# Performance work log

Measured on AMD Instinct MI355X. Metric: run time of the kernel, lower is better.

Reference implementation:

```python
import jax, jax.numpy as jnp
import numpy as np

H = 512          # hidden_dim
T = 20           # output_seq_len
EPS = 1e-5


def _ln(x, g, b):
    m = jnp.mean(x, axis=-1, keepdims=True)
    v = jnp.mean((x - m) ** 2, axis=-1, keepdims=True)
    return (x - m) * jax.lax.rsqrt(v + EPS) * g + b


def setup_inputs() -> dict:
    key = jax.random.key(0)
    ks = jax.random.split(key, 20)
    N, LD, PD = 65536, 128, 32
    s = 0.02
    return {
        "z_q": jax.random.normal(ks[0], (N, LD), jnp.float32),
        "f_prior": jax.random.normal(ks[1], (N, PD), jnp.float32),
        # init_mlp: Linear(160 -> 1024) -> LN -> GELU -> Linear(1024 -> 512) -> Tanh
        "W1": jax.random.normal(ks[2], (LD + PD, 2 * H), jnp.float32) * s,
        "b1": jnp.zeros((2 * H,), jnp.float32),
        "g1": jnp.ones((2 * H,), jnp.float32),
        "be1": jnp.zeros((2 * H,), jnp.float32),
        "W2": jax.random.normal(ks[3], (2 * H, H), jnp.float32) * s,
        "b2": jnp.zeros((H,), jnp.float32),
        # start token (output_dim = 1)
        "start_token": jax.random.normal(ks[4], (1,), jnp.float32) * 0.1,
        # GRU, input_size=1, hidden_size=H, gates stacked [r, z, n] (torch layout)
        "W_ih": jax.random.normal(ks[5], (3 * H, 1), jnp.float32) * s,
        "W_hh": jax.random.normal(ks[6], (3 * H, H), jnp.float32) * s,
        "b_ih": jnp.zeros((3 * H,), jnp.float32),
        "b_hh": jnp.zeros((3 * H,), jnp.float32),
        # output_mlp: Linear(H -> H//2) -> LN -> GELU -> Linear(H//2 -> 1)
        "Wo1": jax.random.normal(ks[7], (H, H // 2), jnp.float32) * s,
        "bo1": jnp.zeros((H // 2,), jnp.float32),
        "go": jnp.ones((H // 2,), jnp.float32),
        "beo": jnp.zeros((H // 2,), jnp.float32),
        "Wo2": jax.random.normal(ks[8], (H // 2, 1), jnp.float32) * s,
        "bo2": jnp.zeros((1,), jnp.float32),
    }


def reference(z_q, f_prior, W1, b1, g1, be1, W2, b2, start_token,
              W_ih, W_hh, b_ih, b_hh, Wo1, bo1, go, beo, Wo2, bo2):
    N = z_q.shape[0]
    # init_mlp -> h_0 (dropout is identity at eval)
    combined = jnp.concatenate([z_q, f_prior], axis=1)          # (N, LD+PD)
    h = jnp.tanh(jax.nn.gelu(_ln(combined @ W1 + b1, g1, be1), approximate=False) @ W2 + b2)  # (N, H)

    x0 = jnp.broadcast_to(start_token[None, :], (N, 1))          # (N, 1)

    def step(carry, _):
        h, x = carry
        gi = x @ W_ih.T + b_ih                                   # (N, 3H)
        gh = h @ W_hh.T + b_hh                                   # (N, 3H)
        r = jax.nn.sigmoid(gi[:, :H] + gh[:, :H])
        z = jax.nn.sigmoid(gi[:, H:2 * H] + gh[:, H:2 * H])
        n = jnp.tanh(gi[:, 2 * H:] + r * gh[:, 2 * H:])
        h_new = (1.0 - z) * n + z * h
        y = jax.nn.gelu(_ln(h_new @ Wo1 + bo1, go, beo), approximate=False) @ Wo2 + bo2  # (N, 1)
        return (h_new, y), y

    _, ys = jax.lax.scan(step, (h, x0), None, length=T)          # (T, N, 1)
    preds = jnp.transpose(ys[..., 0], (1, 0))                    # (N, T), output_dim==1 squeeze
    return preds
```

## Files before the change

kernel.cpp:

```cpp
#include <hip/hip_runtime.h>
#include <math.h>


typedef _Float16 f16;
typedef _Float16 f16x4 __attribute__((ext_vector_type(4)));
typedef _Float16 f16x8 __attribute__((ext_vector_type(8)));
typedef float f32x4 __attribute__((ext_vector_type(4)));

#define TSTEPS 20

__device__ __forceinline__ float sigm(float v) { return 1.0f / (1.0f + __expf(-v)); }
__device__ __forceinline__ float tanh_s(float v) {
  float e = __expf(-2.0f * fabsf(v));
  float r = (1.0f - e) / (1.0f + e);
  return copysignf(r, v);
}
__device__ __forceinline__ float gelu_e(float v) {
  return 0.5f * v * (1.0f + erff(v * 0.70710678118654752f));
}
__device__ __forceinline__ void st4(float* d, float4 v) {
  d[0] = v.x; d[1] = v.y; d[2] = v.z; d[3] = v.w;
}

__device__ __forceinline__ int fa(int m, int k) {
  return (((k >> 5) * 4 + (m >> 4)) << 10) + (((m & 15) + ((k >> 3) & 3) * 16) << 4) + ((k & 7) * 2);
}

__global__ void cvt_weights(const float* __restrict__ W1, const float* __restrict__ W2,
                            const float* __restrict__ Whh, const float* __restrict__ Wo1,
                            const float* __restrict__ bih, const float* __restrict__ bhh,
                            f16* __restrict__ w1t, f16* __restrict__ w2t,
                            f16* __restrict__ whh, f16* __restrict__ wo1t,
                            float* __restrict__ bcr, float* __restrict__ bcz) {
  int i = blockIdx.x * 256 + threadIdx.x;
  if (i < 163840) { int n = i / 160; int k = i - n * 160; w1t[i] = (f16)W1[k * 1024 + n]; return; }
  i -= 163840;
  if (i < 524288) { int n = i >> 10; int k = i & 1023; w2t[i] = (f16)W2[k * 512 + n]; return; }
  i -= 524288;
  if (i < 786432) { whh[i] = (f16)Whh[i]; return; }
  i -= 786432;
  if (i < 131072) { int o = i >> 9; int k = i & 511; wo1t[i] = (f16)Wo1[k * 256 + o]; return; }
  i -= 131072;
  if (i < 512) { bcr[i] = bih[i] + bhh[i]; return; }
  i -= 512;
  if (i < 512) { bcz[i] = bih[512 + i] + bhh[512 + i]; return; }
}

__global__ __launch_bounds__(512, 2)
void gru_main(
    const float* __restrict__ zq, const float* __restrict__ fpr,
    const float* __restrict__ b1, const float* __restrict__ g1, const float* __restrict__ be1,
    const float* __restrict__ b2, const float* __restrict__ stok,
    const float* __restrict__ Wih, const float* __restrict__ bih, const float* __restrict__ bhh,
    const float* __restrict__ bo1, const float* __restrict__ go, const float* __restrict__ beo,
    const float* __restrict__ Wo2, const float* __restrict__ bo2,
    const f16* __restrict__ w1t, const f16* __restrict__ w2t,
    const f16* __restrict__ whh, const f16* __restrict__ wo1t,
    const float* __restrict__ bcr, const float* __restrict__ bcz,
    float* __restrict__ out) {
  __shared__ __align__(16) unsigned char sm[131072];
  __shared__ float sm_s[256], sm_ss[256], sm_yp[256];
  __shared__ float sm_x[64];

  const int tid = threadIdx.x;
  const int w = tid >> 6;
  const int lane = tid & 63;
  const int l16 = lane & 15;
  const int l4 = lane >> 4;
  const int R0 = blockIdx.x * 64;

  const float bo2v = bo2[0];
  if (tid < 64) sm_x[tid] = stok[0];

  #pragma unroll 1
  for (int p = 0; p < 4; ++p) {
    #pragma unroll 1
    for (int jh = 0; jh < 2; ++jh) {
      const int jq0 = w * 128 + p * 32 + jh * 16;
      f32x4 acc[4];
      #pragma unroll
      for (int mt = 0; mt < 4; ++mt) acc[mt] = (f32x4){0.f, 0.f, 0.f, 0.f};
      #pragma unroll
      for (int kf = 0; kf < 5; ++kf) {
        const int k0 = kf * 32 + l4 * 8;
        f16x8 B[4];
        #pragma unroll
        for (int mt = 0; mt < 4; ++mt) {
          const int gm = R0 + mt * 16 + l16;
          const float* src = (kf < 4) ? (zq + gm * 128 + k0) : (fpr + gm * 32 + (k0 - 128));
          float4 v0 = *(const float4*)src;
          float4 v1 = *(const float4*)(src + 4);
          f16x8 b;
          b[0] = (f16)v0.x; b[1] = (f16)v0.y; b[2] = (f16)v0.z; b[3] = (f16)v0.w;
          b[4] = (f16)v1.x; b[5] = (f16)v1.y; b[6] = (f16)v1.z; b[7] = (f16)v1.w;
          B[mt] = b;
        }
        const f16x8 A = *(const f16x8*)(w1t + (jq0 + l16) * 160 + k0);
        #pragma unroll
        for (int mt = 0; mt < 4; ++mt)
          acc[mt] = __builtin_amdgcn_mfma_f32_16x16x32_f16(A, B[mt], acc[mt], 0, 0, 0);
      }
      const int jq = jq0 + l4 * 4;
      float bb[4]; st4(bb, *(const float4*)(b1 + jq));
      #pragma unroll
      for (int mt = 0; mt < 4; ++mt) {
        f16x4 v;
        #pragma unroll
        for (int r = 0; r < 4; ++r) v[r] = (f16)(acc[mt][r] + bb[r]);
        *(f16x4*)(sm + fa(mt * 16 + l16, jq)) = v;
      }
    }
  }
  __syncthreads();
  {
    const int mt = w & 3, half = w >> 2;
    const int row = mt * 16 + l16;
    float s = 0.f, ss = 0.f;
    #pragma unroll 4
    for (int it = 0; it < 16; ++it) {
      const int kb = half * 16 + it;
      f16x8 v = *(const f16x8*)(sm + (kb * 4 + mt) * 1024 + lane * 16);
      #pragma unroll
      for (int i = 0; i < 8; ++i) { float f = (float)v[i]; s += f; ss += f * f; }
    }
    s += __shfl_xor(s, 16); ss += __shfl_xor(ss, 16);
    s += __shfl_xor(s, 32); ss += __shfl_xor(ss, 32);
    if (l4 == 0) { sm_s[row * 2 + half] = s; sm_ss[row * 2 + half] = ss; }
    __syncthreads();
    const float mean = (sm_s[row * 2] + sm_s[row * 2 + 1]) * (1.f / 1024.f);
    const float q2 = (sm_ss[row * 2] + sm_ss[row * 2 + 1]) * (1.f / 1024.f);
    const float rstd = rsqrtf(q2 - mean * mean + 1e-5f);
    #pragma unroll 2
    for (int it = 0; it < 16; ++it) {
      const int kb = half * 16 + it;
      const int off = (kb * 4 + mt) * 1024 + lane * 16;
      const int c = kb * 32 + l4 * 8;
      f16x8 v = *(const f16x8*)(sm + off);
      float4 ga = *(const float4*)(g1 + c);
      float4 gb = *(const float4*)(g1 + c + 4);
      float4 ba = *(const float4*)(be1 + c);
      float4 bb = *(const float4*)(be1 + c + 4);
      float gs[8] = {ga.x, ga.y, ga.z, ga.w, gb.x, gb.y, gb.z, gb.w};
      float bs[8] = {ba.x, ba.y, ba.z, ba.w, bb.x, bb.y, bb.z, bb.w};
      f16x8 o;
      #pragma unroll
      for (int i = 0; i < 8; ++i)
        o[i] = (f16)gelu_e(((float)v[i] - mean) * rstd * gs[i] + bs[i]);
      *(f16x8*)(sm + off) = o;
    }
  }
  __syncthreads();
  f16x4 hold[4][4];
  #pragma unroll 1
  for (int pp = 0; pp < 4; ++pp) {
    const int jq0 = w * 64 + pp * 16;
    f32x4 acc[4];
    #pragma unroll
    for (int mt = 0; mt < 4; ++mt) acc[mt] = (f32x4){0.f, 0.f, 0.f, 0.f};
    #pragma unroll 2
    for (int kf = 0; kf < 32; ++kf) {
      f16x8 B[4];
      #pragma unroll
      for (int mt = 0; mt < 4; ++mt)
        B[mt] = *(const f16x8*)(sm + (kf * 4 + mt) * 1024 + lane * 16);
      const f16x8 A = *(const f16x8*)(w2t + (jq0 + l16) * 1024 + kf * 32 + l4 * 8);
      #pragma unroll
      for (int mt = 0; mt < 4; ++mt)
        acc[mt] = __builtin_amdgcn_mfma_f32_16x16x32_f16(A, B[mt], acc[mt], 0, 0, 0);
    }
    const int jq = jq0 + l4 * 4;
    float bb[4]; st4(bb, *(const float4*)(b2 + jq));
    #pragma unroll
    for (int mt = 0; mt < 4; ++mt) {
      f16x4 v;
      #pragma unroll
      for (int r = 0; r < 4; ++r) v[r] = (f16)tanh_s(acc[mt][r] + bb[r]);
      hold[pp][mt] = v;
    }
  }
  __syncthreads();
  #pragma unroll
  for (int pp = 0; pp < 4; ++pp) {
    const int jq = w * 64 + pp * 16 + l4 * 4;
    #pragma unroll
    for (int mt = 0; mt < 4; ++mt)
      *(f16x4*)(sm + fa(mt * 16 + l16, jq)) = hold[pp][mt];
  }
  __syncthreads();

  #pragma unroll 1
  for (int t = 0; t < TSTEPS; ++t) {
    const int cur = (t & 1) << 16;
    const int nxt = cur ^ 65536;
    #pragma unroll 1
    for (int p = 0; p < 2; ++p) {
      f32x4 acc[4][3][2];
      #pragma unroll
      for (int mt = 0; mt < 4; ++mt)
        #pragma unroll
        for (int g = 0; g < 3; ++g)
          #pragma unroll
          for (int jh = 0; jh < 2; ++jh) acc[mt][g][jh] = (f32x4){0.f, 0.f, 0.f, 0.f};
      #pragma unroll 2
      for (int kf = 0; kf < 16; ++kf) {
        f16x8 B[4];
        #pragma unroll
        for (int mt = 0; mt < 4; ++mt)
          B[mt] = *(const f16x8*)(sm + cur + (kf * 4 + mt) * 1024 + lane * 16);
        #pragma unroll
        for (int g = 0; g < 3; ++g)
          #pragma unroll
          for (int jh = 0; jh < 2; ++jh) {
            const f16x8 A = *(const f16x8*)(whh + (g * 512 + w * 64 + p * 32 + jh * 16 + l16) * 512 + kf * 32 + l4 * 8);
            #pragma unroll
            for (int mt = 0; mt < 4; ++mt)
              acc[mt][g][jh] = __builtin_amdgcn_mfma_f32_16x16x32_f16(A, B[mt], acc[mt][g][jh], 0, 0, 0);
          }
      }
      if (p == 0) __syncthreads();
      #pragma unroll
      for (int jh = 0; jh < 2; ++jh) {
        const int jq = w * 64 + p * 32 + jh * 16 + l4 * 4;
        float wr[4], wz[4], wn[4], cr[4], cz[4], bn[4], cn[4];
        st4(wr, *(const float4*)(Wih + jq));
        st4(wz, *(const float4*)(Wih + 512 + jq));
        st4(wn, *(const float4*)(Wih + 1024 + jq));
        st4(cr, *(const float4*)(bcr + jq));
        st4(cz, *(const float4*)(bcz + jq));
        st4(bn, *(const float4*)(bih + 1024 + jq));
        st4(cn, *(const float4*)(bhh + 1024 + jq));
        #pragma unroll
        for (int mt = 0; mt < 4; ++mt) {
          const int m = mt * 16 + l16;
          const float x = sm_x[m];
          const int hoff = fa(m, jq);
          const f16x4 ho = *(const f16x4*)(sm + cur + hoff);
          f16x4 hn;
          #pragma unroll
          for (int r = 0; r < 4; ++r) {
            const float gr = sigm(x * wr[r] + cr[r] + acc[mt][0][jh][r]);
            const float gz = sigm(x * wz[r] + cz[r] + acc[mt][1][jh][r]);
            const float gn = tanh_s(x * wn[r] + bn[r] + gr * (acc[mt][2][jh][r] + cn[r]));
            hn[r] = (f16)((1.f - gz) * gn + gz * (float)ho[r]);
          }
          *(f16x4*)(sm + nxt + hoff) = hn;
        }
      }
    }
    __syncthreads();
    {
      const int mg = w >> 2, jg = w & 3;
      f32x4 a2[2][4];
      #pragma unroll
      for (int mi = 0; mi < 2; ++mi)
        #pragma unroll
        for (int jt2 = 0; jt2 < 4; ++jt2) a2[mi][jt2] = (f32x4){0.f, 0.f, 0.f, 0.f};
      #pragma unroll 2
      for (int kf = 0; kf < 16; ++kf) {
        f16x8 B[2];
        #pragma unroll
        for (int mi = 0; mi < 2; ++mi)
          B[mi] = *(const f16x8*)(sm + nxt + (kf * 4 + mg * 2 + mi) * 1024 + lane * 16);
        #pragma unroll
        for (int jt2 = 0; jt2 < 4; ++jt2) {
          const f16x8 A = *(const f16x8*)(wo1t + (jg * 64 + jt2 * 16 + l16) * 512 + kf * 32 + l4 * 8);
          #pragma unroll
          for (int mi = 0; mi < 2; ++mi)
            a2[mi][jt2] = __builtin_amdgcn_mfma_f32_16x16x32_f16(A, B[mi], a2[mi][jt2], 0, 0, 0);
        }
      }
      float vv[2][4][4];
      float bo1v[4][4];
      #pragma unroll
      for (int jt2 = 0; jt2 < 4; ++jt2)
        st4(bo1v[jt2], *(const float4*)(bo1 + jg * 64 + jt2 * 16 + l4 * 4));
      #pragma unroll
      for (int mi = 0; mi < 2; ++mi) {
        float s = 0.f, ss = 0.f;
        #pragma unroll
        for (int jt2 = 0; jt2 < 4; ++jt2)
          #pragma unroll
          for (int r = 0; r < 4; ++r) {
            const float v = a2[mi][jt2][r] + bo1v[jt2][r];
            vv[mi][jt2][r] = v; s += v; ss += v * v;
          }
        s += __shfl_xor(s, 16); ss += __shfl_xor(ss, 16);
        s += __shfl_xor(s, 32); ss += __shfl_xor(ss, 32);
        if (l4 == 0) {
          const int m = (mg * 2 + mi) * 16 + l16;
          sm_s[m * 4 + jg] = s;
          sm_ss[m * 4 + jg] = ss;
        }
      }
      __syncthreads();
      float gov[4][4], bev[4][4], wv[4][4];
      #pragma unroll
      for (int jt2 = 0; jt2 < 4; ++jt2) {
        const int jb = jg * 64 + jt2 * 16 + l4 * 4;
        st4(gov[jt2], *(const float4*)(go + jb));
        st4(bev[jt2], *(const float4*)(beo + jb));
        st4(wv[jt2], *(const float4*)(Wo2 + jb));
      }
      #pragma unroll
      for (int mi = 0; mi < 2; ++mi) {
        const int m = (mg * 2 + mi) * 16 + l16;
        float4 ps = *(const float4*)(sm_s + m * 4);
        float4 pq = *(const float4*)(sm_ss + m * 4);
        const float mean = (ps.x + ps.y + ps.z + ps.w) * (1.f / 256.f);
        const float q2 = (pq.x + pq.y + pq.z + pq.w) * (1.f / 256.f);
        const float rstd = rsqrtf(q2 - mean * mean + 1e-5f);
        float y = 0.f;
        #pragma unroll
        for (int jt2 = 0; jt2 < 4; ++jt2)
          #pragma unroll
          for (int r = 0; r < 4; ++r)
            y += gelu_e((vv[mi][jt2][r] - mean) * rstd * gov[jt2][r] + bev[jt2][r]) * wv[jt2][r];
        y += __shfl_xor(y, 16);
        y += __shfl_xor(y, 32);
        if (l4 == 0) sm_yp[m * 4 + jg] = y;
      }
      __syncthreads();
      if (tid < 64) {
        float4 ps = *(const float4*)(sm_yp + tid * 4);
        const float y = bo2v + ps.x + ps.y + ps.z + ps.w;
        sm_x[tid] = y;
        out[(R0 + tid) * 20 + t] = y;
      }
    }
  }
}

extern "C" void kernel_launch(void* const* d_in, const int* in_sizes, int n_in,
                              void* d_out, int out_size, void* d_ws, size_t ws_size,
                              hipStream_t stream) {
  const float* zq   = (const float*)d_in[0];
  const float* fpr  = (const float*)d_in[1];
  const float* W1   = (const float*)d_in[2];
  const float* b1   = (const float*)d_in[3];
  const float* g1   = (const float*)d_in[4];
  const float* be1  = (const float*)d_in[5];
  const float* W2   = (const float*)d_in[6];
  const float* b2   = (const float*)d_in[7];
  const float* stok = (const float*)d_in[8];
  const float* Wih  = (const float*)d_in[9];
  const float* Whh  = (const float*)d_in[10];
  const float* bih  = (const float*)d_in[11];
  const float* bhh  = (const float*)d_in[12];
  const float* Wo1  = (const float*)d_in[13];
  const float* bo1  = (const float*)d_in[14];
  const float* go   = (const float*)d_in[15];
  const float* beo  = (const float*)d_in[16];
  const float* Wo2  = (const float*)d_in[17];
  const float* bo2  = (const float*)d_in[18];

  char* ws = (char*)d_ws;
  f16* w1t   = (f16*)(ws + 0);
  f16* w2t   = (f16*)(ws + 327680);
  f16* whh   = (f16*)(ws + 1376256);
  f16* wo1t  = (f16*)(ws + 2949120);
  float* bcr = (float*)(ws + 3211264);
  float* bcz = (float*)(ws + 3213312);

  cvt_weights<<<6276, 256, 0, stream>>>(W1, W2, Whh, Wo1, bih, bhh,
                                        w1t, w2t, whh, wo1t, bcr, bcz);

  const int N = in_sizes[0] / 128;
  gru_main<<<N / 64, 512, 0, stream>>>(zq, fpr, b1, g1, be1, b2, stok, Wih, bih, bhh,
                                       bo1, go, beo, Wo2, bo2, w1t, w2t, whh, wo1t,
                                       bcr, bcz, (float*)d_out);
}
```

Measured before the change: 5.997 ms.

## Halve shared memory by splitting init MLP into row halves and single-buffering h

After: 7.707 ms. 1.29x slower.

```diff
diff --git a/kernel.cpp b/kernel.cpp
--- a/kernel.cpp
+++ b/kernel.cpp
@@ -25,13 +25,17 @@
 __device__ __forceinline__ int fa(int m, int k) {
   return (((k >> 5) * 4 + (m >> 4)) << 10) + (((m & 15) + ((k >> 3) & 3) * 16) << 4) + ((k & 7) * 2);
 }
+__device__ __forceinline__ int fa32(int m, int k) {
+  return (((k >> 5) * 2 + ((m >> 4) & 1)) << 10) + (((m & 15) + ((k >> 3) & 3) * 16) << 4) + ((k & 7) * 2);
+}
 
 __global__ void cvt_weights(const float* __restrict__ W1, const float* __restrict__ W2,
                             const float* __restrict__ Whh, const float* __restrict__ Wo1,
-                            const float* __restrict__ bih, const float* __restrict__ bhh,
+                            const float* __restrict__ Wih, const float* __restrict__ bih,
+                            const float* __restrict__ bhh,
                             f16* __restrict__ w1t, f16* __restrict__ w2t,
                             f16* __restrict__ whh, f16* __restrict__ wo1t,
-                            float* __restrict__ bcr, float* __restrict__ bcz) {
+                            f16* __restrict__ c7) {
   int i = blockIdx.x * 256 + threadIdx.x;
   if (i < 163840) { int n = i / 160; int k = i - n * 160; w1t[i] = (f16)W1[k * 1024 + n]; return; }
   i -= 163840;
@@ -41,9 +45,18 @@
   i -= 786432;
   if (i < 131072) { int o = i >> 9; int k = i & 511; wo1t[i] = (f16)Wo1[k * 256 + o]; return; }
   i -= 131072;
-  if (i < 512) { bcr[i] = bih[i] + bhh[i]; return; }
-  i -= 512;
-  if (i < 512) { bcz[i] = bih[512 + i] + bhh[512 + i]; return; }
+  if (i < 3584) {
+    const int which = i >> 9, j = i & 511;
+    float v;
+    if (which == 0) v = Wih[j];
+    else if (which == 1) v = Wih[512 + j];
+    else if (which == 2) v = Wih[1024 + j];
+    else if (which == 3) v = bih[j] + bhh[j];
+    else if (which == 4) v = bih[512 + j] + bhh[512 + j];
+    else if (which == 5) v = bih[1024 + j];
+    else v = bhh[1024 + j];
+    c7[i] = (f16)v;
+  }
 }
 
 __global__ __launch_bounds__(512, 2)
@@ -51,14 +64,13 @@
     const float* __restrict__ zq, const float* __restrict__ fpr,
     const float* __restrict__ b1, const float* __restrict__ g1, const float* __restrict__ be1,
     const float* __restrict__ b2, const float* __restrict__ stok,
-    const float* __restrict__ Wih, const float* __restrict__ bih, const float* __restrict__ bhh,
     const float* __restrict__ bo1, const float* __restrict__ go, const float* __restrict__ beo,
     const float* __restrict__ Wo2, const float* __restrict__ bo2,
     const f16* __restrict__ w1t, const f16* __restrict__ w2t,
     const f16* __restrict__ whh, const f16* __restrict__ wo1t,
-    const float* __restrict__ bcr, const float* __restrict__ bcz,
+    const f16* __restrict__ c7,
     float* __restrict__ out) {
-  __shared__ __align__(16) unsigned char sm[131072];
+  __shared__ __align__(16) unsigned char sm[65536];
   __shared__ float sm_s[256], sm_ss[256], sm_yp[256];
   __shared__ float sm_x[64];
 
@@ -72,180 +84,199 @@
   const float bo2v = bo2[0];
   if (tid < 64) sm_x[tid] = stok[0];
 
-  #pragma unroll 1
-  for (int p = 0; p < 4; ++p) {
+  f16x4 h0h[2][4][2];
+
+  #pragma unroll
+  for (int hh = 0; hh < 2; ++hh) {
+    const int RH = R0 + hh * 32;
     #pragma unroll 1
-    for (int jh = 0; jh < 2; ++jh) {
-      const int jq0 = w * 128 + p * 32 + jh * 16;
-      f32x4 acc[4];
-      #pragma unroll
-      for (int mt = 0; mt < 4; ++mt) acc[mt] = (f32x4){0.f, 0.f, 0.f, 0.f};
-      #pragma unroll
-      for (int kf = 0; kf < 5; ++kf) {
-        const int k0 = kf * 32 + l4 * 8;
-        f16x8 B[4];
-        #pragma unroll
-        for (int mt = 0; mt < 4; ++mt) {
-          const int gm = R0 + mt * 16 + l16;
-          const float* src = (kf < 4) ? (zq + gm * 128 + k0) : (fpr + gm * 32 + (k0 - 128));
-          float4 v0 = *(const float4*)src;
-          float4 v1 = *(const float4*)(src + 4);
-          f16x8 b;
-          b[0] = (f16)v0.x; b[1] = (f16)v0.y; b[2] = (f16)v0.z; b[3] = (f16)v0.w;
-          b[4] = (f16)v1.x; b[5] = (f16)v1.y; b[6] = (f16)v1.z; b[7] = (f16)v1.w;
-          B[mt] = b;
-        }
-        const f16x8 A = *(const f16x8*)(w1t + (jq0 + l16) * 160 + k0);
-        #pragma unroll
-        for (int mt = 0; mt < 4; ++mt)
+    for (int p = 0; p < 4; ++p) {
+      #pragma unroll 1
+      for (int jh = 0; jh < 2; ++jh) {
+        const int jq0 = w * 128 + p * 32 + jh * 16;
+        f32x4 acc[2];
+        #pragma unroll
+        for (int mt = 0; mt < 2; ++mt) acc[mt] = (f32x4){0.f, 0.f, 0.f, 0.f};
+        #pragma unroll
+        for (int kf = 0; kf < 5; ++kf) {
+          const int k0 = kf * 32 + l4 * 8;
+          f16x8 B[2];
+          #pragma unroll
+          for (int mt = 0; mt < 2; ++mt) {
+            const int gm = RH + mt * 16 + l16;
+            const float* src = (kf < 4) ? (zq + gm * 128 + k0) : (fpr + gm * 32 + (k0 - 128));
+            float4 v0 = *(const float4*)src;
+            float4 v1 = *(const float4*)(src + 4);
+            f16x8 b;
+            b[0] = (f16)v0.x; b[1] = (f16)v0.y; b[2] = (f16)v0.z; b[3] = (f16)v0.w;
+            b[4] = (f16)v1.x; b[5] = (f16)v1.y; b[6] = (f16)v1.z; b[7] = (f16)v1.w;
+            B[mt] = b;
+          }
+          const f16x8 A = *(const f16x8*)(w1t + (jq0 + l16) * 160 + k0);
+          #pragma unroll
+          for (int mt = 0; mt < 2; ++mt)
+            acc[mt] = __builtin_amdgcn_mfma_f32_16x16x32_f16(A, B[mt], acc[mt], 0, 0, 0);
+        }
+        const int jq = jq0 + l4 * 4;
+        float bb[4]; st4(bb, *(const float4*)(b1 + jq));
+        #pragma unroll
+        for (int mt = 0; mt < 2; ++mt) {
+          f16x4 v;
+          #pragma unroll
+          for (int r = 0; r < 4; ++r) v[r] = (f16)(acc[mt][r] + bb[r]);
+          *(f16x4*)(sm + fa32(mt * 16 + l16, jq)) = v;
+        }
+      }
+    }
+    __syncthreads();
+    {
+      float s0 = 0.f, q0 = 0.f, s1 = 0.f, q1 = 0.f;
+      #pragma unroll
+      for (int i = 0; i < 8; ++i) {
+        f16x8 v = *(const f16x8*)(sm + (w * 8 + i) * 1024 + lane * 16);
+        float ls = 0.f, lq = 0.f;
+        #pragma unroll
+        for (int j = 0; j < 8; ++j) { float f = (float)v[j]; ls += f; lq += f * f; }
+        if (i & 1) { s1 += ls; q1 += lq; } else { s0 += ls; q0 += lq; }
+      }
+      s0 += __shfl_xor(s0, 16); q0 += __shfl_xor(q0, 16);
+      s0 += __shfl_xor(s0, 32); q0 += __shfl_xor(q0, 32);
+      s1 += __shfl_xor(s1, 16); q1 += __shfl_xor(q1, 16);
+      s1 += __shfl_xor(s1, 32); q1 += __shfl_xor(q1, 32);
+      if (l4 == 0) {
+        sm_s[l16 * 8 + w] = s0;        sm_ss[l16 * 8 + w] = q0;
+        sm_s[(16 + l16) * 8 + w] = s1; sm_ss[(16 + l16) * 8 + w] = q1;
+      }
+      __syncthreads();
+      float mean[2], rstd[2];
+      #pragma unroll
+      for (int mt = 0; mt < 2; ++mt) {
+        const int row = mt * 16 + l16;
+        float s = 0.f, q = 0.f;
+        #pragma unroll
+        for (int i = 0; i < 8; ++i) { s += sm_s[row * 8 + i]; q += sm_ss[row * 8 + i]; }
+        mean[mt] = s * (1.f / 1024.f);
+        rstd[mt] = rsqrtf(q * (1.f / 1024.f) - mean[mt] * mean[mt] + 1e-5f);
+      }
+      #pragma unroll 2
+      for (int i = 0; i < 8; ++i) {
+        const int chunk = w * 8 + i;
+        const int off = chunk * 1024 + lane * 16;
+        const int c = (chunk >> 1) * 32 + l4 * 8;
+        const int mt = i & 1;
+        f16x8 v = *(const f16x8*)(sm + off);
+        float4 ga = *(const float4*)(g1 + c);
+        float4 gb = *(const float4*)(g1 + c + 4);
+        float4 ba = *(const float4*)(be1 + c);
+        float4 bb = *(const float4*)(be1 + c + 4);
+        float gs[8] = {ga.x, ga.y, ga.z, ga.w, gb.x, gb.y, gb.z, gb.w};
+        float bs[8] = {ba.x, ba.y, ba.z, ba.w, bb.x, bb.y, bb.z, bb.w};
+        f16x8 o;
+        #pragma unroll
+        for (int j = 0; j < 8; ++j)
+          o[j] = (f16)gelu_e(((float)v[j] - mean[mt]) * rstd[mt] * gs[j] + bs[j]);
+        *(f16x8*)(sm + off) = o;
+      }
+    }
+    __syncthreads();
+    #pragma unroll
+    for (int pp = 0; pp < 4; ++pp) {
+      const int jq0 = w * 64 + pp * 16;
+      f32x4 acc[2];
+      #pragma unroll
+      for (int mt = 0; mt < 2; ++mt) acc[mt] = (f32x4){0.f, 0.f, 0.f, 0.f};
+      #pragma unroll 2
+      for (int kf = 0; kf < 32; ++kf) {
+        f16x8 B[2];
+        #pragma unroll
+        for (int mt = 0; mt < 2; ++mt)
+          B[mt] = *(const f16x8*)(sm + (kf * 2 + mt) * 1024 + lane * 16);
+        const f16x8 A = *(const f16x8*)(w2t + (jq0 + l16) * 1024 + kf * 32 + l4 * 8);
+        #pragma unroll
+        for (int mt = 0; mt < 2; ++mt)
           acc[mt] = __builtin_amdgcn_mfma_f32_16x16x32_f16(A, B[mt], acc[mt], 0, 0, 0);
       }
       const int jq = jq0 + l4 * 4;
-      float bb[4]; st4(bb, *(const float4*)(b1 + jq));
-      #pragma unroll
-      for (int mt = 0; mt < 4; ++mt) {
+      float bb[4]; st4(bb, *(const float4*)(b2 + jq));
+      #pragma unroll
+      for (int mt = 0; mt < 2; ++mt) {
         f16x4 v;
         #pragma unroll
-        for (int r = 0; r < 4; ++r) v[r] = (f16)(acc[mt][r] + bb[r]);
-        *(f16x4*)(sm + fa(mt * 16 + l16, jq)) = v;
-      }
-    }
+        for (int r = 0; r < 4; ++r) v[r] = (f16)tanh_s(acc[mt][r] + bb[r]);
+        h0h[hh][pp][mt] = v;
+      }
+    }
+    __syncthreads();
   }
-  __syncthreads();
-  {
-    const int mt = w & 3, half = w >> 2;
-    const int row = mt * 16 + l16;
-    float s = 0.f, ss = 0.f;
-    #pragma unroll 4
-    for (int it = 0; it < 16; ++it) {
-      const int kb = half * 16 + it;
-      f16x8 v = *(const f16x8*)(sm + (kb * 4 + mt) * 1024 + lane * 16);
-      #pragma unroll
-      for (int i = 0; i < 8; ++i) { float f = (float)v[i]; s += f; ss += f * f; }
-    }
-    s += __shfl_xor(s, 16); ss += __shfl_xor(ss, 16);
-    s += __shfl_xor(s, 32); ss += __shfl_xor(ss, 32);
-    if (l4 == 0) { sm_s[row * 2 + half] = s; sm_ss[row * 2 + half] = ss; }
-    __syncthreads();
-    const float mean = (sm_s[row * 2] + sm_s[row * 2 + 1]) * (1.f / 1024.f);
-    const float q2 = (sm_ss[row * 2] + sm_ss[row * 2 + 1]) * (1.f / 1024.f);
-    const float rstd = rsqrtf(q2 - mean * mean + 1e-5f);
-    #pragma unroll 2
-    for (int it = 0; it < 16; ++it) {
-      const int kb = half * 16 + it;
-      const int off = (kb * 4 + mt) * 1024 + lane * 16;
-      const int c = kb * 32 + l4 * 8;
-      f16x8 v = *(const f16x8*)(sm + off);
-      float4 ga = *(const float4*)(g1 + c);
-      float4 gb = *(const float4*)(g1 + c + 4);
-      float4 ba = *(const float4*)(be1 + c);
-      float4 bb = *(const float4*)(be1 + c + 4);
-      float gs[8] = {ga.x, ga.y, ga.z, ga.w, gb.x, gb.y, gb.z, gb.w};
-      float bs[8] = {ba.x, ba.y, ba.z, ba.w, bb.x, bb.y, bb.z, bb.w};
-      f16x8 o;
-      #pragma unroll
-      for (int i = 0; i < 8; ++i)
-        o[i] = (f16)gelu_e(((float)v[i] - mean) * rstd * gs[i] + bs[i]);
-      *(f16x8*)(sm + off) = o;
-    }
-  }
-  __syncthreads();
-  f16x4 hold[4][4];
-  #pragma unroll 1
-  for (int pp = 0; pp < 4; ++pp) {
-    const int jq0 = w * 64 + pp * 16;
-    f32x4 acc[4];
+  #pragma unroll
+  for (int hh = 0; hh < 2; ++hh)
     #pragma unroll
-    for (int mt = 0; mt < 4; ++mt) acc[mt] = (f32x4){0.f, 0.f, 0.f, 0.f};
-    #pragma unroll 2
-    for (int kf = 0; kf < 32; ++kf) {
-      f16x8 B[4];
-      #pragma unroll
-      for (int mt = 0; mt < 4; ++mt)
-        B[mt] = *(const f16x8*)(sm + (kf * 4 + mt) * 1024 + lane * 16);
-      const f16x8 A = *(const f16x8*)(w2t + (jq0 + l16) * 1024 + kf * 32 + l4 * 8);
-      #pragma unroll
-      for (int mt = 0; mt < 4; ++mt)
-        acc[mt] = __builtin_amdgcn_mfma_f32_16x16x32_f16(A, B[mt], acc[mt], 0, 0, 0);
-    }
-    const int jq = jq0 + l4 * 4;
-    float bb[4]; st4(bb, *(const float4*)(b2 + jq));
-    #pragma unroll
-    for (int mt = 0; mt < 4; ++mt) {
-      f16x4 v;
-      #pragma unroll
-      for (int r = 0; r < 4; ++r) v[r] = (f16)tanh_s(acc[mt][r] + bb[r]);
-      hold[pp][mt] = v;
-    }
-  }
-  __syncthreads();
-  #pragma unroll
-  for (int pp = 0; pp < 4; ++pp) {
-    const int jq = w * 64 + pp * 16 + l4 * 4;
-    #pragma unroll
-    for (int mt = 0; mt < 4; ++mt)
-      *(f16x4*)(sm + fa(mt * 16 + l16, jq)) = hold[pp][mt];
-  }
+    for (int pp = 0; pp < 4; ++pp) {
+      const int jq = w * 64 + pp * 16 + l4 * 4;
+      #pragma unroll
+      for (int mt = 0; mt < 2; ++mt)
+        *(f16x4*)(sm + fa(hh * 32 + mt * 16 + l16, jq)) = h0h[hh][pp][mt];
+    }
   __syncthreads();
 
   #pragma unroll 1
   for (int t = 0; t < TSTEPS; ++t) {
-    const int cur = (t & 1) << 16;
-    const int nxt = cur ^ 65536;
-    #pragma unroll 1
-    for (int p = 0; p < 2; ++p) {
-      f32x4 acc[4][3][2];
+    f16x4 hnh[4][4];
+    #pragma unroll
+    for (int q = 0; q < 4; ++q) {
+      const int jt = w * 64 + q * 16;
+      f32x4 acc[4][3];
       #pragma unroll
       for (int mt = 0; mt < 4; ++mt)
         #pragma unroll
-        for (int g = 0; g < 3; ++g)
-          #pragma unroll
-          for (int jh = 0; jh < 2; ++jh) acc[mt][g][jh] = (f32x4){0.f, 0.f, 0.f, 0.f};
+        for (int g = 0; g < 3; ++g) acc[mt][g] = (f32x4){0.f, 0.f, 0.f, 0.f};
       #pragma unroll 2
       for (int kf = 0; kf < 16; ++kf) {
         f16x8 B[4];
         #pragma unroll
         for (int mt = 0; mt < 4; ++mt)
-          B[mt] = *(const f16x8*)(sm + cur + (kf * 4 + mt) * 1024 + lane * 16);
-        #pragma unroll
-        for (int g = 0; g < 3; ++g)
-          #pragma unroll
-          for (int jh = 0; jh < 2; ++jh) {
-            const f16x8 A = *(const f16x8*)(whh + (g * 512 + w * 64 + p * 32 + jh * 16 + l16) * 512 + kf * 32 + l4 * 8);
-            #pragma unroll
-            for (int mt = 0; mt < 4; ++mt)
-              acc[mt][g][jh] = __builtin_amdgcn_mfma_f32_16x16x32_f16(A, B[mt], acc[mt][g][jh], 0, 0, 0);
-          }
-      }
-      if (p == 0) __syncthreads();
-      #pragma unroll
-      for (int jh = 0; jh < 2; ++jh) {
-        const int jq = w * 64 + p * 32 + jh * 16 + l4 * 4;
-        float wr[4], wz[4], wn[4], cr[4], cz[4], bn[4], cn[4];
-        st4(wr, *(const float4*)(Wih + jq));
-        st4(wz, *(const float4*)(Wih + 512 + jq));
-        st4(wn, *(const float4*)(Wih + 1024 + jq));
-        st4(cr, *(const float4*)(bcr + jq));
-        st4(cz, *(const float4*)(bcz + jq));
-        st4(bn, *(const float4*)(bih + 1024 + jq));
-        st4(cn, *(const float4*)(bhh + 1024 + jq));
-        #pragma unroll
-        for (int mt = 0; mt < 4; ++mt) {
-          const int m = mt * 16 + l16;
-          const float x = sm_x[m];
-          const int hoff = fa(m, jq);
-          const f16x4 ho = *(const f16x4*)(sm + cur + hoff);
-          f16x4 hn;
-          #pragma unroll
-          for (int r = 0; r < 4; ++r) {
-            const float gr = sigm(x * wr[r] + cr[r] + acc[mt][0][jh][r]);
-            const float gz = sigm(x * wz[r] + cz[r] + acc[mt][1][jh][r]);
-            const float gn = tanh_s(x * wn[r] + bn[r] + gr * (acc[mt][2][jh][r] + cn[r]));
-            hn[r] = (f16)((1.f - gz) * gn + gz * (float)ho[r]);
-          }
-          *(f16x4*)(sm + nxt + hoff) = hn;
-        }
-      }
+          B[mt] = *(const f16x8*)(sm + (kf * 4 + mt) * 1024 + lane * 16);
+        #pragma unroll
+        for (int g = 0; g < 3; ++g) {
+          const f16x8 A = *(const f16x8*)(whh + (g * 512 + jt + l16) * 512 + kf * 32 + l4 * 8);
+          #pragma unroll
+          for (int mt = 0; mt < 4; ++mt)
+            acc[mt][g] = __builtin_amdgcn_mfma_f32_16x16x32_f16(A, B[mt], acc[mt][g], 0, 0, 0);
+        }
+      }
+      if (q == 0) __syncthreads();
+      const int jq = jt + l4 * 4;
+      const f16x4 wrh = *(const f16x4*)(c7 + jq);
+      const f16x4 wzh = *(const f16x4*)(c7 + 512 + jq);
+      const f16x4 wnh = *(const f16x4*)(c7 + 1024 + jq);
+      const f16x4 crh = *(const f16x4*)(c7 + 1536 + jq);
+      const f16x4 czh = *(const f16x4*)(c7 + 2048 + jq);
+      const f16x4 bnh = *(const f16x4*)(c7 + 2560 + jq);
+      const f16x4 cnh = *(const f16x4*)(c7 + 3072 + jq);
+      #pragma unroll
+      for (int mt = 0; mt < 4; ++mt) {
+        const int m = mt * 16 + l16;
+        const float x = sm_x[m];
+        const int hoff = fa(m, jq);
+        const f16x4 ho = *(const f16x4*)(sm + hoff);
+        f16x4 hn;
+        #pragma unroll
+        for (int r = 0; r < 4; ++r) {
+          const float gr = sigm(x * (float)wrh[r] + (float)crh[r] + acc[mt][0][r]);
+          const float gz = sigm(x * (float)wzh[r] + (float)czh[r] + acc[mt][1][r]);
+          const float gn = tanh_s(x * (float)wnh[r] + (float)bnh[r] + gr * (acc[mt][2][r] + (float)cnh[r]));
+          hn[r] = (f16)((1.f - gz) * gn + gz * (float)ho[r]);
+        }
+        hnh[q][mt] = hn;
+      }
+    }
+    __syncthreads();
+    #pragma unroll
+    for (int q = 0; q < 4; ++q) {
+      const int jq = w * 64 + q * 16 + l4 * 4;
+      #pragma unroll
+      for (int mt = 0; mt < 4; ++mt)
+        *(f16x4*)(sm + fa(mt * 16 + l16, jq)) = hnh[q][mt];
     }
     __syncthreads();
     {
@@ -260,7 +291,7 @@
         f16x8 B[2];
         #pragma unroll
         for (int mi = 0; mi < 2; ++mi)
-          B[mi] = *(const f16x8*)(sm + nxt + (kf * 4 + mg * 2 + mi) * 1024 + lane * 16);
+          B[mi] = *(const f16x8*)(sm + (kf * 4 + mg * 2 + mi) * 1024 + lane * 16);
         #pragma unroll
         for (int jt2 = 0; jt2 < 4; ++jt2) {
           const f16x8 A = *(const f16x8*)(wo1t + (jg * 64 + jt2 * 16 + l16) * 512 + kf * 32 + l4 * 8);
@@ -354,18 +385,17 @@
   const float* bo2  = (const float*)d_in[18];
 
   char* ws = (char*)d_ws;
-  f16* w1t   = (f16*)(ws + 0);
-  f16* w2t   = (f16*)(ws + 327680);
-  f16* whh   = (f16*)(ws + 1376256);
-  f16* wo1t  = (f16*)(ws + 2949120);
-  float* bcr = (float*)(ws + 3211264);
-  float* bcz = (float*)(ws + 3213312);
-
-  cvt_weights<<<6276, 256, 0, stream>>>(W1, W2, Whh, Wo1, bih, bhh,
-                                        w1t, w2t, whh, wo1t, bcr, bcz);
+  f16* w1t  = (f16*)(ws + 0);
+  f16* w2t  = (f16*)(ws + 327680);
+  f16* whh  = (f16*)(ws + 1376256);
+  f16* wo1t = (f16*)(ws + 2949120);
+  f16* c7   = (f16*)(ws + 3211264);
+
+  cvt_weights<<<6287, 256, 0, stream>>>(W1, W2, Whh, Wo1, Wih, bih, bhh,
+                                        w1t, w2t, whh, wo1t, c7);
 
   const int N = in_sizes[0] / 128;
-  gru_main<<<N / 64, 512, 0, stream>>>(zq, fpr, b1, g1, be1, b2, stok, Wih, bih, bhh,
-                                       bo1, go, beo, Wo2, bo2, w1t, w2t, whh, wo1t,
-                                       bcr, bcz, (float*)d_out);
-}
+  gru_main<<<N / 64, 512, 0, stream>>>(zq, fpr, b1, g1, be1, b2, stok,
+                                       bo1, go, beo, Wo2, bo2,
+                                       w1t, w2t, whh, wo1t, c7, (float*)d_out);
+}
```

## Prefetch MFMA weight fragments one k-step ahead and stage GRU constants in LDS

Applied to the files above, without the earlier changes.

Measured after the change: 5.262 ms. 1.14x faster.

```diff
diff --git a/kernel.cpp b/kernel.cpp
--- a/kernel.cpp
+++ b/kernel.cpp
@@ -28,10 +28,11 @@
 
 __global__ void cvt_weights(const float* __restrict__ W1, const float* __restrict__ W2,
                             const float* __restrict__ Whh, const float* __restrict__ Wo1,
-                            const float* __restrict__ bih, const float* __restrict__ bhh,
+                            const float* __restrict__ Wih, const float* __restrict__ bih,
+                            const float* __restrict__ bhh,
                             f16* __restrict__ w1t, f16* __restrict__ w2t,
                             f16* __restrict__ whh, f16* __restrict__ wo1t,
-                            float* __restrict__ bcr, float* __restrict__ bcz) {
+                            f16* __restrict__ c7) {
   int i = blockIdx.x * 256 + threadIdx.x;
   if (i < 163840) { int n = i / 160; int k = i - n * 160; w1t[i] = (f16)W1[k * 1024 + n]; return; }
   i -= 163840;
@@ -41,9 +42,18 @@
   i -= 786432;
   if (i < 131072) { int o = i >> 9; int k = i & 511; wo1t[i] = (f16)Wo1[k * 256 + o]; return; }
   i -= 131072;
-  if (i < 512) { bcr[i] = bih[i] + bhh[i]; return; }
-  i -= 512;
-  if (i < 512) { bcz[i] = bih[512 + i] + bhh[512 + i]; return; }
+  if (i < 3584) {
+    const int which = i >> 9, j = i & 511;
+    float v;
+    if (which == 0) v = Wih[j];
+    else if (which == 1) v = Wih[512 + j];
+    else if (which == 2) v = Wih[1024 + j];
+    else if (which == 3) v = bih[j] + bhh[j];
+    else if (which == 4) v = bih[512 + j] + bhh[512 + j];
+    else if (which == 5) v = bih[1024 + j];
+    else v = bhh[1024 + j];
+    c7[i] = (f16)v;
+  }
 }
 
 __global__ __launch_bounds__(512, 2)
@@ -51,16 +61,17 @@
     const float* __restrict__ zq, const float* __restrict__ fpr,
     const float* __restrict__ b1, const float* __restrict__ g1, const float* __restrict__ be1,
     const float* __restrict__ b2, const float* __restrict__ stok,
-    const float* __restrict__ Wih, const float* __restrict__ bih, const float* __restrict__ bhh,
     const float* __restrict__ bo1, const float* __restrict__ go, const float* __restrict__ beo,
     const float* __restrict__ Wo2, const float* __restrict__ bo2,
     const f16* __restrict__ w1t, const f16* __restrict__ w2t,
     const f16* __restrict__ whh, const f16* __restrict__ wo1t,
-    const float* __restrict__ bcr, const float* __restrict__ bcz,
+    const f16* __restrict__ c7,
     float* __restrict__ out) {
   __shared__ __align__(16) unsigned char sm[131072];
   __shared__ float sm_s[256], sm_ss[256], sm_yp[256];
   __shared__ float sm_x[64];
+  __shared__ __align__(8) f16 sm_c7[3584];
+  __shared__ __align__(16) float sm_aux[1024];
 
   const int tid = threadIdx.x;
   const int w = tid >> 6;
@@ -71,6 +82,10 @@
 
   const float bo2v = bo2[0];
   if (tid < 64) sm_x[tid] = stok[0];
+  for (int i = tid; i < 1792; i += 512)
+    ((unsigned*)sm_c7)[i] = ((const unsigned*)c7)[i];
+  for (int i = tid; i < 1024; i += 512)
+    sm_aux[i] = (i < 256) ? bo1[i] : (i < 512) ? go[i - 256] : (i < 768) ? beo[i - 512] : Wo2[i - 768];
 
   #pragma unroll 1
   for (int p = 0; p < 4; ++p) {
@@ -144,31 +159,45 @@
       float bs[8] = {ba.x, ba.y, ba.z, ba.w, bb.x, bb.y, bb.z, bb.w};
       f16x8 o;
       #pragma unroll
-      for (int i = 0; i < 8; ++i)
-        o[i] = (f16)gelu_e(((float)v[i] - mean) * rstd * gs[i] + bs[i]);
+      for (int j = 0; j < 8; ++j)
+        o[j] = (f16)gelu_e(((float)v[j] - mean) * rstd * gs[j] + bs[j]);
       *(f16x8*)(sm + off) = o;
     }
   }
   __syncthreads();
   f16x4 hold[4][4];
-  #pragma unroll 1
+  #pragma unroll
   for (int pp = 0; pp < 4; ++pp) {
-    const int jq0 = w * 64 + pp * 16;
+    const f16* Ab = w2t + (w * 64 + pp * 16 + l16) * 1024 + l4 * 8;
     f32x4 acc[4];
     #pragma unroll
     for (int mt = 0; mt < 4; ++mt) acc[mt] = (f32x4){0.f, 0.f, 0.f, 0.f};
-    #pragma unroll 2
-    for (int kf = 0; kf < 32; ++kf) {
-      f16x8 B[4];
-      #pragma unroll
-      for (int mt = 0; mt < 4; ++mt)
-        B[mt] = *(const f16x8*)(sm + (kf * 4 + mt) * 1024 + lane * 16);
-      const f16x8 A = *(const f16x8*)(w2t + (jq0 + l16) * 1024 + kf * 32 + l4 * 8);
-      #pragma unroll
-      for (int mt = 0; mt < 4; ++mt)
-        acc[mt] = __builtin_amdgcn_mfma_f32_16x16x32_f16(A, B[mt], acc[mt], 0, 0, 0);
-    }
-    const int jq = jq0 + l4 * 4;
+    f16x8 A0 = *(const f16x8*)(Ab);
+    f16x8 A1 = *(const f16x8*)(Ab + 32);
+    #pragma unroll 1
+    for (int kp = 0; kp < 16; ++kp) {
+      {
+        f16x8 B[4];
+        #pragma unroll
+        for (int mt = 0; mt < 4; ++mt)
+          B[mt] = *(const f16x8*)(sm + ((kp * 8 + mt) << 10) + lane * 16);
+        #pragma unroll
+        for (int mt = 0; mt < 4; ++mt)
+          acc[mt] = __builtin_amdgcn_mfma_f32_16x16x32_f16(A0, B[mt], acc[mt], 0, 0, 0);
+        if (kp < 15) A0 = *(const f16x8*)(Ab + (kp * 2 + 2) * 32);
+      }
+      {
+        f16x8 B[4];
+        #pragma unroll
+        for (int mt = 0; mt < 4; ++mt)
+          B[mt] = *(const f16x8*)(sm + ((kp * 8 + 4 + mt) << 10) + lane * 16);
+        #pragma unroll
+        for (int mt = 0; mt < 4; ++mt)
+          acc[mt] = __builtin_amdgcn_mfma_f32_16x16x32_f16(A1, B[mt], acc[mt], 0, 0, 0);
+        if (kp < 15) A1 = *(const f16x8*)(Ab + (kp * 2 + 3) * 32);
+      }
+    }
+    const int jq = w * 64 + pp * 16 + l4 * 4;
     float bb[4]; st4(bb, *(const float4*)(b2 + jq));
     #pragma unroll
     for (int mt = 0; mt < 4; ++mt) {
@@ -193,87 +222,134 @@
     const int cur = (t & 1) << 16;
     const int nxt = cur ^ 65536;
     #pragma unroll 1
-    for (int p = 0; p < 2; ++p) {
-      f32x4 acc[4][3][2];
+    for (int q = 0; q < 4; ++q) {
+      const int jt = w * 64 + q * 16;
+      const f16* Ab = whh + (jt + l16) * 512 + l4 * 8;
+      f32x4 acc[4][3];
       #pragma unroll
       for (int mt = 0; mt < 4; ++mt)
         #pragma unroll
-        for (int g = 0; g < 3; ++g)
-          #pragma unroll
-          for (int jh = 0; jh < 2; ++jh) acc[mt][g][jh] = (f32x4){0.f, 0.f, 0.f, 0.f};
-      #pragma unroll 2
-      for (int kf = 0; kf < 16; ++kf) {
-        f16x8 B[4];
-        #pragma unroll
-        for (int mt = 0; mt < 4; ++mt)
-          B[mt] = *(const f16x8*)(sm + cur + (kf * 4 + mt) * 1024 + lane * 16);
-        #pragma unroll
-        for (int g = 0; g < 3; ++g)
-          #pragma unroll
-          for (int jh = 0; jh < 2; ++jh) {
-            const f16x8 A = *(const f16x8*)(whh + (g * 512 + w * 64 + p * 32 + jh * 16 + l16) * 512 + kf * 32 + l4 * 8);
+        for (int g = 0; g < 3; ++g) acc[mt][g] = (f32x4){0.f, 0.f, 0.f, 0.f};
+      f16x8 A0[3], A1[3];
+      #pragma unroll
+      for (int g = 0; g < 3; ++g) A0[g] = *(const f16x8*)(Ab + g * 262144);
+      #pragma unroll
+      for (int g = 0; g < 3; ++g) A1[g] = *(const f16x8*)(Ab + g * 262144 + 32);
+      #pragma unroll 1
+      for (int kp = 0; kp < 8; ++kp) {
+        {
+          f16x8 B[4];
+          #pragma unroll
+          for (int mt = 0; mt < 4; ++mt)
+            B[mt] = *(const f16x8*)(sm + cur + ((kp * 8 + mt) << 10) + lane * 16);
+          #pragma unroll
+          for (int g = 0; g < 3; ++g)
             #pragma unroll
             for (int mt = 0; mt < 4; ++mt)
-              acc[mt][g][jh] = __builtin_amdgcn_mfma_f32_16x16x32_f16(A, B[mt], acc[mt][g][jh], 0, 0, 0);
+              acc[mt][g] = __builtin_amdgcn_mfma_f32_16x16x32_f16(A0[g], B[mt], acc[mt][g], 0, 0, 0);
+          if (kp < 7) {
+            #pragma unroll
+            for (int g = 0; g < 3; ++g)
+              A0[g] = *(const f16x8*)(Ab + g * 262144 + (kp * 2 + 2) * 32);
           }
-      }
-      if (p == 0) __syncthreads();
-      #pragma unroll
-      for (int jh = 0; jh < 2; ++jh) {
-        const int jq = w * 64 + p * 32 + jh * 16 + l4 * 4;
-        float wr[4], wz[4], wn[4], cr[4], cz[4], bn[4], cn[4];
-        st4(wr, *(const float4*)(Wih + jq));
-        st4(wz, *(const float4*)(Wih + 512 + jq));
-        st4(wn, *(const float4*)(Wih + 1024 + jq));
-        st4(cr, *(const float4*)(bcr + jq));
-        st4(cz, *(const float4*)(bcz + jq));
-        st4(bn, *(const float4*)(bih + 1024 + jq));
-        st4(cn, *(const float4*)(bhh + 1024 + jq));
-        #pragma unroll
-        for (int mt = 0; mt < 4; ++mt) {
-          const int m = mt * 16 + l16;
-          const float x = sm_x[m];
-          const int hoff = fa(m, jq);
-          const f16x4 ho = *(const f16x4*)(sm + cur + hoff);
-          f16x4 hn;
-          #pragma unroll
-          for (int r = 0; r < 4; ++r) {
-            const float gr = sigm(x * wr[r] + cr[r] + acc[mt][0][jh][r]);
-            const float gz = sigm(x * wz[r] + cz[r] + acc[mt][1][jh][r]);
-            const float gn = tanh_s(x * wn[r] + bn[r] + gr * (acc[mt][2][jh][r] + cn[r]));
-            hn[r] = (f16)((1.f - gz) * gn + gz * (float)ho[r]);
+        }
+        {
+          f16x8 B[4];
+          #pragma unroll
+          for (int mt = 0; mt < 4; ++mt)
+            B[mt] = *(const f16x8*)(sm + cur + ((kp * 8 + 4 + mt) << 10) + lane * 16);
+          #pragma unroll
+          for (int g = 0; g < 3; ++g)
+            #pragma unroll
+            for (int mt = 0; mt < 4; ++mt)
+              acc[mt][g] = __builtin_amdgcn_mfma_f32_16x16x32_f16(A1[g], B[mt], acc[mt][g], 0, 0, 0);
+          if (kp < 7) {
+            #pragma unroll
+            for (int g = 0; g < 3; ++g)
+              A1[g] = *(const f16x8*)(Ab + g * 262144 + (kp * 2 + 3) * 32);
           }
-          *(f16x4*)(sm + nxt + hoff) = hn;
-        }
+        }
+      }
+      if (q == 0) __syncthreads();
+      const int jq = jt + l4 * 4;
+      const f16x4 wrh = *(const f16x4*)(sm_c7 + jq);
+      const f16x4 wzh = *(const f16x4*)(sm_c7 + 512 + jq);
+      const f16x4 wnh = *(const f16x4*)(sm_c7 + 1024 + jq);
+      const f16x4 crh = *(const f16x4*)(sm_c7 + 1536 + jq);
+      const f16x4 czh = *(const f16x4*)(sm_c7 + 2048 + jq);
+      const f16x4 bnh = *(const f16x4*)(sm_c7 + 2560 + jq);
+      const f16x4 cnh = *(const f16x4*)(sm_c7 + 3072 + jq);
+      #pragma unroll
+      for (int mt = 0; mt < 4; ++mt) {
+        const int m = mt * 16 + l16;
+        const float x = sm_x[m];
+        const int hoff = fa(m, jq);
+        const f16x4 ho = *(const f16x4*)(sm + cur + hoff);
+        f16x4 hn;
+        #pragma unroll
+        for (int r = 0; r < 4; ++r) {
+          const float gr = sigm(x * (float)wrh[r] + (float)crh[r] + acc[mt][0][r]);
+          const float gz = sigm(x * (float)wzh[r] + (float)czh[r] + acc[mt][1][r]);
+          const float gn = tanh_s(x * (float)wnh[r] + (float)bnh[r] + gr * (acc[mt][2][r] + (float)cnh[r]));
+          hn[r] = (f16)((1.f - gz) * gn + gz * (float)ho[r]);
+        }
+        *(f16x4*)(sm + nxt + hoff) = hn;
       }
     }
     __syncthreads();
     {
       const int mg = w >> 2, jg = w & 3;
+      const f16* Ab2 = wo1t + (jg * 64 + l16) * 512 + l4 * 8;
       f32x4 a2[2][4];
       #pragma unroll
       for (int mi = 0; mi < 2; ++mi)
         #pragma unroll
         for (int jt2 = 0; jt2 < 4; ++jt2) a2[mi][jt2] = (f32x4){0.f, 0.f, 0.f, 0.f};
-      #pragma unroll 2
-      for (int kf = 0; kf < 16; ++kf) {
-        f16x8 B[2];
-        #pragma unroll
-        for (int mi = 0; mi < 2; ++mi)
-          B[mi] = *(const f16x8*)(sm + nxt + (kf * 4 + mg * 2 + mi) * 1024 + lane * 16);
-        #pragma unroll
-        for (int jt2 = 0; jt2 < 4; ++jt2) {
-          const f16x8 A = *(const f16x8*)(wo1t + (jg * 64 + jt2 * 16 + l16) * 512 + kf * 32 + l4 * 8);
+      f16x8 C0[4], C1[4];
+      #pragma unroll
+      for (int jt2 = 0; jt2 < 4; ++jt2) C0[jt2] = *(const f16x8*)(Ab2 + jt2 * 8192);
+      #pragma unroll
+      for (int jt2 = 0; jt2 < 4; ++jt2) C1[jt2] = *(const f16x8*)(Ab2 + jt2 * 8192 + 32);
+      #pragma unroll 1
+      for (int kp = 0; kp < 8; ++kp) {
+        {
+          f16x8 B[2];
           #pragma unroll
           for (int mi = 0; mi < 2; ++mi)
-            a2[mi][jt2] = __builtin_amdgcn_mfma_f32_16x16x32_f16(A, B[mi], a2[mi][jt2], 0, 0, 0);
+            B[mi] = *(const f16x8*)(sm + nxt + ((kp * 8 + mg * 2 + mi) << 10) + lane * 16);
+          #pragma unroll
+          for (int jt2 = 0; jt2 < 4; ++jt2)
+            #pragma unroll
+            for (int mi = 0; mi < 2; ++mi)
+              a2[mi][jt2] = __builtin_amdgcn_mfma_f32_16x16x32_f16(C0[jt2], B[mi], a2[mi][jt2], 0, 0, 0);
+          if (kp < 7) {
+            #pragma unroll
+            for (int jt2 = 0; jt2 < 4; ++jt2)
+              C0[jt2] = *(const f16x8*)(Ab2 + jt2 * 8192 + (kp * 2 + 2) * 32);
+          }
+        }
+        {
+          f16x8 B[2];
+          #pragma unroll
+          for (int mi = 0; mi < 2; ++mi)
+            B[mi] = *(const f16x8*)(sm + nxt + ((kp * 8 + 4 + mg * 2 + mi) << 10) + lane * 16);
+          #pragma unroll
+          for (int jt2 = 0; jt2 < 4; ++jt2)
+            #pragma unroll
+            for (int mi = 0; mi < 2; ++mi)
+              a2[mi][jt2] = __builtin_amdgcn_mfma_f32_16x16x32_f16(C1[jt2], B[mi], a2[mi][jt2], 0, 0, 0);
+          if (kp < 7) {
+            #pragma unroll
+            for (int jt2 = 0; jt2 < 4; ++jt2)
+              C1[jt2] = *(const f16x8*)(Ab2 + jt2 * 8192 + (kp * 2 + 3) * 32);
+          }
         }
       }
       float vv[2][4][4];
       float bo1v[4][4];
       #pragma unroll
       for (int jt2 = 0; jt2 < 4; ++jt2)
-        st4(bo1v[jt2], *(const float4*)(bo1 + jg * 64 + jt2 * 16 + l4 * 4));
+        st4(bo1v[jt2], *(const float4*)(sm_aux + jg * 64 + jt2 * 16 + l4 * 4));
       #pragma unroll
       for (int mi = 0; mi < 2; ++mi) {
         float s = 0.f, ss = 0.f;
@@ -297,9 +373,9 @@
       #pragma unroll
       for (int jt2 = 0; jt2 < 4; ++jt2) {
         const int jb = jg * 64 + jt2 * 16 + l4 * 4;
-        st4(gov[jt2], *(const float4*)(go + jb));
-        st4(bev[jt2], *(const float4*)(beo + jb));
-        st4(wv[jt2], *(const float4*)(Wo2 + jb));
+        st4(gov[jt2], *(const float4*)(sm_aux + 256 + jb));
+        st4(bev[jt2], *(const float4*)(sm_aux + 512 + jb));
+        st4(wv[jt2], *(const float4*)(sm_aux + 768 + jb));
       }
       #pragma unroll
       for (int mi = 0; mi < 2; ++mi) {
@@ -354,18 +430,17 @@
   const float* bo2  = (const float*)d_in[18];
 
   char* ws = (char*)d_ws;
-  f16* w1t   = (f16*)(ws + 0);
-  f16* w2t   = (f16*)(ws + 327680);
-  f16* whh   = (f16*)(ws + 1376256);
-  f16* wo1t  = (f16*)(ws + 2949120);
-  float* bcr = (float*)(ws + 3211264);
-  float* bcz = (float*)(ws + 3213312);
-
-  cvt_weights<<<6276, 256, 0, stream>>>(W1, W2, Whh, Wo1, bih, bhh,
-                                        w1t, w2t, whh, wo1t, bcr, bcz);
+  f16* w1t  = (f16*)(ws + 0);
+  f16* w2t  = (f16*)(ws + 327680);
+  f16* whh  = (f16*)(ws + 1376256);
+  f16* wo1t = (f16*)(ws + 2949120);
+  f16* c7   = (f16*)(ws + 3211264);
+
+  cvt_weights<<<6287, 256, 0, stream>>>(W1, W2, Whh, Wo1, Wih, bih, bhh,
+                                        w1t, w2t, whh, wo1t, c7);
 
   const int N = in_sizes[0] / 128;
-  gru_main<<<N / 64, 512, 0, stream>>>(zq, fpr, b1, g1, be1, b2, stok, Wih, bih, bhh,
-                                       bo1, go, beo, Wo2, bo2, w1t, w2t, whh, wo1t,
-                                       bcr, bcz, (float*)d_out);
-}
+  gru_main<<<N / 64, 512, 0, stream>>>(zq, fpr, b1, g1, be1, b2, stok,
+                                       bo1, go, beo, Wo2, bo2,
+                                       w1t, w2t, whh, wo1t, c7, (float*)d_out);
+}
```
